# Optimization experiments

Hardware: AMD Instinct MI355X
Metric: run time of the kernel (lower is better)

Reference implementation:

```python
import jax, jax.numpy as jnp
import numpy as np

# Config constants (from cfg in init_kwargs)
B = 4            # batch size (num point clouds)
V = 80000        # total pillars across batch
P = 20           # max points per pillar
C_IN = 4         # x, y, z, intensity
C_OUT = 64       # PillarFeatureNet output channels
NY = NX = 640    # BEV grid
BEV_M = 100.0    # bev_range_m per axis
Z_CUT = 5.0
VX = BEV_M / NX              # 0.15625 m
VY = BEV_M / NY
X_OFF = VX / 2.0 - BEV_M / 2.0   # voxel-center offset, pc_range_min + vx/2
Y_OFF = VY / 2.0 - BEV_M / 2.0
BN_EPS = 1e-3


def setup_inputs() -> dict:
    key = jax.random.key(0)
    k1, k2, k3, k4 = jax.random.split(key, 4)
    # points: xy in [-50, 50), z in [-5, 5), intensity in [0, 1)
    xy = jax.random.uniform(k1, (V, P, 2), jnp.float32, -BEV_M / 2, BEV_M / 2)
    z = jax.random.uniform(k2, (V, P, 1), jnp.float32, -Z_CUT, Z_CUT)
    intensity = jax.random.uniform(k3, (V, P, 1), jnp.float32)
    voxels = jnp.concatenate([xy, z, intensity], axis=-1)  # [V, P, 4]
    num_points = jax.random.randint(k4, (V,), 1, P + 1).astype(jnp.int32)
    # unique pillar coordinates (hard voxelization never emits duplicates)
    rng = np.random.default_rng(0)
    flat = rng.choice(B * NY * NX, size=V, replace=False).astype(np.int32)
    b = flat // (NY * NX)
    rem = flat % (NY * NX)
    y = rem // NX
    x = rem % NX
    coors = jnp.asarray(np.stack([b, np.zeros_like(b), y, x], axis=-1))  # [V,4] (b,z,y,x)
    # PFN layer params: Linear(9->64, bias=False) + BN1d(64)
    W = jax.random.normal(jax.random.fold_in(key, 10), (9, C_OUT), jnp.float32) * 0.05
    gamma = jnp.ones((C_OUT,), jnp.float32)
    beta = jnp.zeros((C_OUT,), jnp.float32)
    running_mean = jnp.zeros((C_OUT,), jnp.float32)
    running_var = jnp.ones((C_OUT,), jnp.float32)
    return {"voxels": voxels, "num_points": num_points, "coors": coors,
            "W": W, "gamma": gamma, "beta": beta,
            "running_mean": running_mean, "running_var": running_var}


def reference(voxels, num_points, coors, W, gamma, beta, running_mean, running_var):
    dt = voxels.dtype
    xyz = voxels[..., :3]                                       # [V,P,3]
    npts = jnp.maximum(num_points, 1).astype(dt)[:, None, None]
    # cluster-center offsets (mean over valid points; padded slots are zero here,
    # matching hard voxelization which zero-pads)
    valid = (jnp.arange(P)[None, :] < num_points[:, None])      # [V,P] bool
    xyz_m = xyz * valid[..., None].astype(dt)
    f_cluster = xyz - jnp.sum(xyz_m, axis=1, keepdims=True) / npts
    # voxel-center offsets (xy only, legacy PillarFeatureNet)
    cx = coors[:, 3].astype(dt)[:, None, None] * VX + X_OFF
    cy = coors[:, 2].astype(dt)[:, None, None] * VY + Y_OFF
    f_center = jnp.concatenate([voxels[..., 0:1] - cx, voxels[..., 1:2] - cy], axis=-1)
    feats = jnp.concatenate([voxels, f_cluster, f_center], axis=-1)  # [V,P,9]
    feats = feats * valid[..., None].astype(dt)
    # PFN layer: linear -> BN1d (eval, running stats) -> relu -> max over points
    h = jnp.einsum('vpi,io->vpo', feats, W)                     # [V,P,64]
    h = (h - running_mean) * jax.lax.rsqrt(running_var + BN_EPS) * gamma + beta
    h = jax.nn.relu(h)
    pillar_feats = jnp.max(h, axis=1)                           # [V,64]
    # scatter to dense BEV canvas [B, C, NY, NX]
    flat = coors[:, 0] * (NY * NX) + coors[:, 2] * NX + coors[:, 3]  # [V]
    canvas = jnp.zeros((B * NY * NX, C_OUT), dt).at[flat].set(pillar_feats)
    canvas = canvas.reshape(B, NY, NX, C_OUT).transpose(0, 3, 1, 2)
    occ = jnp.zeros((B * NY * NX, 1), dt).at[flat].set(jnp.ones((V, 1), dt))
    occ = occ.reshape(B, NY, NX, 1).transpose(0, 3, 1, 2)
    return canvas, occ
```

## Files before the change

### kernel.cpp

```cpp
#include <hip/hip_runtime.h>

constexpr int B_    = 4;
constexpr int V_    = 80000;
constexpr int P_    = 20;
constexpr int COUT  = 64;
constexpr int NX_   = 640;
constexpr int NY_   = 640;
constexpr int NYX   = NX_ * NY_;
constexpr float BEV = 100.0f;
constexpr float VXc = BEV / NX_;
constexpr float VYc = BEV / NY_;
constexpr float XOFF = VXc * 0.5f - BEV * 0.5f;
constexpr float YOFF = VYc * 0.5f - BEV * 0.5f;
constexpr float EPS  = 0.001f;

typedef float  vf4 __attribute__((ext_vector_type(4)));

__global__ __launch_bounds__(256) void pillar_feat_kernel(
    const float* __restrict__ voxels,
    const int*   __restrict__ num_points,
    const int*   __restrict__ coors,
    const float* __restrict__ W,
    const float* __restrict__ gamma_,
    const float* __restrict__ beta_,
    const float* __restrict__ rmean,
    const float* __restrict__ rvar,
    float* __restrict__ feat,
    int*   __restrict__ idxmap)
{
    const int v = blockIdx.x * 4 + (threadIdx.x >> 6);
    const int c = threadIdx.x & 63;
    if (v >= V_) return;

    int n = num_points[v];
    n = n < 1 ? 1 : (n > P_ ? P_ : n);

    const int cb  = coors[4 * v + 0];
    const int cyi = coors[4 * v + 2];
    const int cxi = coors[4 * v + 3];

    const float scale = gamma_[c] * rsqrtf(rvar[c] + EPS);
    const float bias  = beta_[c] - rmean[c] * scale;
    float w[9];
    #pragma unroll
    for (int i = 0; i < 9; ++i) w[i] = W[i * COUT + c] * scale;

    const float4* __restrict__ pv =
        (const float4*)(voxels + (size_t)v * (P_ * 4));

    float sx = 0.f, sy = 0.f, sz = 0.f;
    for (int p = 0; p < n; ++p) {
        float4 q = pv[p];
        sx += q.x; sy += q.y; sz += q.z;
    }
    const float inv = 1.0f / (float)n;
    const float mx = sx * inv, my = sy * inv, mz = sz * inv;
    const float ccx = (float)cxi * VXc + XOFF;
    const float ccy = (float)cyi * VYc + YOFF;

    float m = -3.4e38f;
    for (int p = 0; p < n; ++p) {
        float4 q = pv[p];
        float h = bias;
        h += q.x * w[0];
        h += q.y * w[1];
        h += q.z * w[2];
        h += q.w * w[3];
        h += (q.x - mx)  * w[4];
        h += (q.y - my)  * w[5];
        h += (q.z - mz)  * w[6];
        h += (q.x - ccx) * w[7];
        h += (q.y - ccy) * w[8];
        m = fmaxf(m, h);
    }
    if (n < P_) m = fmaxf(m, bias);

    feat[(size_t)v * COUT + c] = fmaxf(m, 0.0f);

    if (c == 0) idxmap[cb * NYX + cyi * NX_ + cxi] = v;
}

__global__ __launch_bounds__(256) void scatter_kernel(
    const float* __restrict__ feat,
    const int*   __restrict__ idxmap,
    float* __restrict__ canvas,
    float* __restrict__ occ)
{
    const int t = blockIdx.x * blockDim.x + threadIdx.x;
    if (t >= (B_ * NYX) / 4) return;

    const int4 id = ((const int4*)idxmap)[t];
    const int cell0 = t * 4;
    const int b   = cell0 / NYX;
    const int rem = cell0 - b * NYX;

    vf4 o = { id.x >= 0 ? 1.f : 0.f,
              id.y >= 0 ? 1.f : 0.f,
              id.z >= 0 ? 1.f : 0.f,
              id.w >= 0 ? 1.f : 0.f };
    __builtin_nontemporal_store(o, (vf4*)(occ + cell0));

    const float4* __restrict__ f4 = (const float4*)feat;
    const size_t base = (size_t)b * COUT * NYX + (size_t)rem;

    #pragma unroll
    for (int cg = 0; cg < 16; ++cg) {
        float4 a0 = make_float4(0.f, 0.f, 0.f, 0.f);
        float4 a1 = a0, a2 = a0, a3 = a0;
        if (id.x >= 0) a0 = f4[(size_t)id.x * 16 + cg];
        if (id.y >= 0) a1 = f4[(size_t)id.y * 16 + cg];
        if (id.z >= 0) a2 = f4[(size_t)id.z * 16 + cg];
        if (id.w >= 0) a3 = f4[(size_t)id.w * 16 + cg];
        vf4 s0 = { a0.x, a1.x, a2.x, a3.x };
        vf4 s1 = { a0.y, a1.y, a2.y, a3.y };
        vf4 s2 = { a0.z, a1.z, a2.z, a3.z };
        vf4 s3 = { a0.w, a1.w, a2.w, a3.w };
        float* p0 = canvas + base + (size_t)(4 * cg + 0) * NYX;
        __builtin_nontemporal_store(s0, (vf4*)p0);
        __builtin_nontemporal_store(s1, (vf4*)(p0 + NYX));
        __builtin_nontemporal_store(s2, (vf4*)(p0 + 2 * NYX));
        __builtin_nontemporal_store(s3, (vf4*)(p0 + 3 * NYX));
    }
}

extern "C" void kernel_launch(void* const* d_in, const int* in_sizes, int n_in,
                              void* d_out, int out_size, void* d_ws, size_t ws_size,
                              hipStream_t stream) {
    const float* voxels     = (const float*)d_in[0];
    const int*   num_points = (const int*)  d_in[1];
    const int*   coors      = (const int*)  d_in[2];
    const float* W          = (const float*)d_in[3];
    const float* gamma_     = (const float*)d_in[4];
    const float* beta_      = (const float*)d_in[5];
    const float* rmean      = (const float*)d_in[6];
    const float* rvar       = (const float*)d_in[7];

    float* canvas = (float*)d_out;
    float* occ    = (float*)d_out + (size_t)B_ * COUT * NYX;

    float* feat   = (float*)d_ws;
    int*   idxmap = (int*)((char*)d_ws + (size_t)V_ * COUT * sizeof(float));

    (void)hipMemsetAsync(idxmap, 0xFF, (size_t)B_ * NYX * sizeof(int), stream);

    pillar_feat_kernel<<<(V_ + 3) / 4, 256, 0, stream>>>(
        voxels, num_points, coors, W, gamma_, beta_, rmean, rvar, feat, idxmap);

    scatter_kernel<<<(B_ * NYX / 4 + 255) / 256, 256, 0, stream>>>(
        feat, idxmap, canvas, occ);
}
```

Measured before the change: 557.7 us.

## Fold per-point affine terms into single pass and drop idxmap memset via validation

```diff
diff --git a/kernel.cpp b/kernel.cpp
--- a/kernel.cpp
+++ b/kernel.cpp
@@ -35,9 +35,8 @@
     int n = num_points[v];
     n = n < 1 ? 1 : (n > P_ ? P_ : n);
 
-    const int cb  = coors[4 * v + 0];
-    const int cyi = coors[4 * v + 2];
-    const int cxi = coors[4 * v + 3];
+    const int4 co = ((const int4*)coors)[v];
+    const int cb = co.x, cyi = co.z, cxi = co.w;
 
     const float scale = gamma_[c] * rsqrtf(rvar[c] + EPS);
     const float bias  = beta_[c] - rmean[c] * scale;
@@ -45,34 +44,29 @@
     #pragma unroll
     for (int i = 0; i < 9; ++i) w[i] = W[i * COUT + c] * scale;
 
+    const float wcx = w[0] + w[4] + w[7];
+    const float wcy = w[1] + w[5] + w[8];
+    const float wcz = w[2] + w[6];
+    const float wcw = w[3];
+
     const float4* __restrict__ pv =
         (const float4*)(voxels + (size_t)v * (P_ * 4));
 
     float sx = 0.f, sy = 0.f, sz = 0.f;
+    float dmax = -3.4e38f;
     for (int p = 0; p < n; ++p) {
         float4 q = pv[p];
         sx += q.x; sy += q.y; sz += q.z;
+        float d = q.x * wcx + q.y * wcy + q.z * wcz + q.w * wcw;
+        dmax = fmaxf(dmax, d);
     }
     const float inv = 1.0f / (float)n;
-    const float mx = sx * inv, my = sy * inv, mz = sz * inv;
     const float ccx = (float)cxi * VXc + XOFF;
     const float ccy = (float)cyi * VYc + YOFF;
+    const float btot = bias - (sx * inv) * w[4] - (sy * inv) * w[5]
+                            - (sz * inv) * w[6] - ccx * w[7] - ccy * w[8];
 
-    float m = -3.4e38f;
-    for (int p = 0; p < n; ++p) {
-        float4 q = pv[p];
-        float h = bias;
-        h += q.x * w[0];
-        h += q.y * w[1];
-        h += q.z * w[2];
-        h += q.w * w[3];
-        h += (q.x - mx)  * w[4];
-        h += (q.y - my)  * w[5];
-        h += (q.z - mz)  * w[6];
-        h += (q.x - ccx) * w[7];
-        h += (q.y - ccy) * w[8];
-        m = fmaxf(m, h);
-    }
+    float m = dmax + btot;
     if (n < P_) m = fmaxf(m, bias);
 
     feat[(size_t)v * COUT + c] = fmaxf(m, 0.0f);
@@ -83,16 +77,28 @@
 __global__ __launch_bounds__(256) void scatter_kernel(
     const float* __restrict__ feat,
     const int*   __restrict__ idxmap,
+    const int*   __restrict__ coors,
     float* __restrict__ canvas,
     float* __restrict__ occ)
 {
     const int t = blockIdx.x * blockDim.x + threadIdx.x;
     if (t >= (B_ * NYX) / 4) return;
 
-    const int4 id = ((const int4*)idxmap)[t];
+    int4 id = ((const int4*)idxmap)[t];
     const int cell0 = t * 4;
     const int b   = cell0 / NYX;
     const int rem = cell0 - b * NYX;
+
+    const int4* __restrict__ co4 = (const int4*)coors;
+    auto check = [&](int idx, int cell) -> int {
+        if (idx < 0 || idx >= V_) return -1;
+        int4 co = co4[idx];
+        return (co.x * NYX + co.z * NX_ + co.w == cell) ? idx : -1;
+    };
+    id.x = check(id.x, cell0 + 0);
+    id.y = check(id.y, cell0 + 1);
+    id.z = check(id.z, cell0 + 2);
+    id.w = check(id.w, cell0 + 3);
 
     vf4 o = { id.x >= 0 ? 1.f : 0.f,
               id.y >= 0 ? 1.f : 0.f,
@@ -141,11 +147,9 @@
     float* feat   = (float*)d_ws;
     int*   idxmap = (int*)((char*)d_ws + (size_t)V_ * COUT * sizeof(float));
 
-    (void)hipMemsetAsync(idxmap, 0xFF, (size_t)B_ * NYX * sizeof(int), stream);
-
     pillar_feat_kernel<<<(V_ + 3) / 4, 256, 0, stream>>>(
         voxels, num_points, coors, W, gamma_, beta_, rmean, rvar, feat, idxmap);
 
     scatter_kernel<<<(B_ * NYX / 4 + 255) / 256, 256, 0, stream>>>(
-        feat, idxmap, canvas, occ);
+        feat, idxmap, coors, canvas, occ);
 }
```

Measured after the change: 514.0 us, median of 2. -7.8%, faster.
